# Optimization experiments

Hardware: AMD Instinct MI355X
Metric: run time of the kernel (lower is better)

## Reference

```python
import jax, jax.numpy as jnp
import numpy as np

IN_FEATURES = 4096
OUT_FEATURES = 11008
N_TOKENS = 32


def setup_inputs() -> dict:
    key = jax.random.key(0)
    k_x, k_w, k_s, k_b = jax.random.split(key, 4)
    x = jax.random.normal(k_x, (N_TOKENS, IN_FEATURES), dtype=jnp.float16)
    # int8 quantized weight, [out_features, in_features]
    qweight = jax.random.randint(k_w, (OUT_FEATURES, IN_FEATURES), -128, 128, dtype=jnp.int8)
    # per-output-channel scales, small positive fp16
    scales = (jax.random.uniform(k_s, (OUT_FEATURES,), dtype=jnp.float32) * 0.01 + 1e-4).astype(jnp.float16)
    bias = (jax.random.normal(k_b, (OUT_FEATURES,), dtype=jnp.float32) * 0.01).astype(jnp.float16)
    return {"x": x, "qweight": qweight, "scales": scales, "bias": bias}


def reference(x, qweight, scales, bias):
    # Dequantize: fp16 weight = int8 * per-row scale  -> [out, in]
    w = (qweight.astype(jnp.float16) * scales[:, None]).astype(jnp.float16)
    # out[t, o] = sum_i x[t, i] * w[o, i]
    out = jnp.einsum("ti,oi->to", x, w) + bias[None, :]
    return out.astype(jnp.float16)
```

## Files before the change

kernel.cpp:

```cpp
#include <hip/hip_runtime.h>
#include <hip/hip_bf16.h>


constexpr int IN_F  = 4096;
constexpr int OUT_F = 11008;

typedef short bf16x8 __attribute__((ext_vector_type(8)));
typedef float f32x4  __attribute__((ext_vector_type(4)));

union B8 { bf16x8 v; unsigned u[4]; };

__device__ __forceinline__ unsigned pack2f(float lo, float hi) {
    return __builtin_amdgcn_perm(__float_as_uint(hi),
                                 __float_as_uint(lo),
                                 0x07060302u);
}

__global__ __launch_bounds__(256, 4)
void qlin_kernel(const float* __restrict__ x,
                 const int* __restrict__ w,
                 const float* __restrict__ scales,
                 const float* __restrict__ bias,
                 float* __restrict__ out)
{
    const int lane = threadIdx.x & 63;
    const int wv   = threadIdx.x >> 6;
    const int r    = lane & 15;
    const int q    = lane >> 4;

    const int n0 = blockIdx.x << 4;
    const int kb = wv << 10;

    f32x4 acc0 = {0.f, 0.f, 0.f, 0.f};
    f32x4 acc1 = {0.f, 0.f, 0.f, 0.f};

    const float* xp0 = x + r * IN_F + kb + q * 8;
    const float* xp1 = xp0 + 16 * IN_F;
    const int* wp = w + (size_t)(n0 + r) * IN_F + kb + q * 8;

    #pragma unroll 2
    for (int kk = 0; kk < 1024; kk += 32) {
        float4 xa = *reinterpret_cast<const float4*>(xp0 + kk);
        float4 xb = *reinterpret_cast<const float4*>(xp0 + kk + 4);
        float4 xc = *reinterpret_cast<const float4*>(xp1 + kk);
        float4 xd = *reinterpret_cast<const float4*>(xp1 + kk + 4);
        int4   qa = *reinterpret_cast<const int4*>(wp + kk);
        int4   qb = *reinterpret_cast<const int4*>(wp + kk + 4);

        B8 a0, a1, bb;
        a0.u[0] = pack2f(xa.x, xa.y);  a0.u[1] = pack2f(xa.z, xa.w);
        a0.u[2] = pack2f(xb.x, xb.y);  a0.u[3] = pack2f(xb.z, xb.w);
        a1.u[0] = pack2f(xc.x, xc.y);  a1.u[1] = pack2f(xc.z, xc.w);
        a1.u[2] = pack2f(xd.x, xd.y);  a1.u[3] = pack2f(xd.z, xd.w);
        bb.u[0] = pack2f((float)qa.x, (float)qa.y);
        bb.u[1] = pack2f((float)qa.z, (float)qa.w);
        bb.u[2] = pack2f((float)qb.x, (float)qb.y);
        bb.u[3] = pack2f((float)qb.z, (float)qb.w);

        acc0 = __builtin_amdgcn_mfma_f32_16x16x32_bf16(a0.v, bb.v, acc0, 0, 0, 0);
        acc1 = __builtin_amdgcn_mfma_f32_16x16x32_bf16(a1.v, bb.v, acc1, 0, 0, 0);
    }

    __shared__ float red[3][2][4][64];
    if (wv > 0) {
        #pragma unroll
        for (int i = 0; i < 4; ++i) {
            red[wv - 1][0][i][lane] = acc0[i];
            red[wv - 1][1][i][lane] = acc1[i];
        }
    }
    __syncthreads();
    if (wv == 0) {
        #pragma unroll
        for (int j = 0; j < 3; ++j) {
            #pragma unroll
            for (int i = 0; i < 4; ++i) {
                acc0[i] += red[j][0][i][lane];
                acc1[i] += red[j][1][i][lane];
            }
        }
        const int n = n0 + r;
        const float s = scales[n];
        const float b = bias[n];
        #pragma unroll
        for (int i = 0; i < 4; ++i) {
            out[(q * 4 + i) * OUT_F + n]      = acc0[i] * s + b;
            out[(16 + q * 4 + i) * OUT_F + n] = acc1[i] * s + b;
        }
    }
}

extern "C" void kernel_launch(void* const* d_in, const int* in_sizes, int n_in,
                              void* d_out, int out_size, void* d_ws, size_t ws_size,
                              hipStream_t stream) {
    const float* x      = (const float*)d_in[0];
    const int*   w      = (const int*)d_in[1];
    const float* scales = (const float*)d_in[2];
    const float* bias   = (const float*)d_in[3];
    float*       out    = (float*)d_out;

    qlin_kernel<<<dim3(OUT_F / 16), dim3(256), 0, stream>>>(x, w, scales, bias, out);
}
```

Baseline: 276.1 us.

## Pre-convert activations to bf16 in a prologue kernel and split K across eight waves

Adds a small kernel that converts x from fp32 to packed bf16 into workspace once. The main kernel then loads bf16 vectors directly instead of re-reading fp32 x and packing it in every block, which halves activation traffic and removes per-block conversion ALU work. Blocks grow to 512 threads with K split across 8 waves, and the LDS reduction widens to 7 partial sums. The cost is an extra kernel launch and a larger cross-wave reduction.

```diff
diff --git a/kernel.cpp b/kernel.cpp
--- a/kernel.cpp
+++ b/kernel.cpp
@@ -2,8 +2,9 @@
 #include <hip/hip_bf16.h>
 
 
-constexpr int IN_F  = 4096;
-constexpr int OUT_F = 11008;
+constexpr int IN_F   = 4096;
+constexpr int OUT_F  = 11008;
+constexpr int KSLICE = IN_F / 8;
 
 typedef short bf16x8 __attribute__((ext_vector_type(8)));
 typedef float f32x4  __attribute__((ext_vector_type(4)));
@@ -16,8 +17,16 @@
                                  0x07060302u);
 }
 
-__global__ __launch_bounds__(256, 4)
-void qlin_kernel(const float* __restrict__ x,
+__global__ __launch_bounds__(256)
+void xconv_kernel(const float* __restrict__ x, unsigned* __restrict__ xb) {
+    const int i = (blockIdx.x * 256 + threadIdx.x) * 4;
+    float4 v = *reinterpret_cast<const float4*>(x + i);
+    xb[i / 2]     = pack2f(v.x, v.y);
+    xb[i / 2 + 1] = pack2f(v.z, v.w);
+}
+
+__global__ __launch_bounds__(512, 4)
+void qlin_kernel(const unsigned short* __restrict__ xb,
                  const int* __restrict__ w,
                  const float* __restrict__ scales,
                  const float* __restrict__ bias,
@@ -29,39 +38,31 @@
     const int q    = lane >> 4;
 
     const int n0 = blockIdx.x << 4;
-    const int kb = wv << 10;
+    const int kb = wv * KSLICE;
 
     f32x4 acc0 = {0.f, 0.f, 0.f, 0.f};
     f32x4 acc1 = {0.f, 0.f, 0.f, 0.f};
 
-    const float* xp0 = x + r * IN_F + kb + q * 8;
-    const float* xp1 = xp0 + 16 * IN_F;
+    const unsigned short* xp0 = xb + r * IN_F + kb + q * 8;
+    const unsigned short* xp1 = xp0 + 16 * IN_F;
     const int* wp = w + (size_t)(n0 + r) * IN_F + kb + q * 8;
 
-    #pragma unroll 2
-    for (int kk = 0; kk < 1024; kk += 32) {
-        float4 xa = *reinterpret_cast<const float4*>(xp0 + kk);
-        float4 xb = *reinterpret_cast<const float4*>(xp0 + kk + 4);
-        float4 xc = *reinterpret_cast<const float4*>(xp1 + kk);
-        float4 xd = *reinterpret_cast<const float4*>(xp1 + kk + 4);
+    #pragma unroll 4
+    for (int kk = 0; kk < KSLICE; kk += 32) {
+        bf16x8 a0 = *reinterpret_cast<const bf16x8*>(xp0 + kk);
+        bf16x8 a1 = *reinterpret_cast<const bf16x8*>(xp1 + kk);
         int4   qa = *reinterpret_cast<const int4*>(wp + kk);
         int4   qb = *reinterpret_cast<const int4*>(wp + kk + 4);
-
-        B8 a0, a1, bb;
-        a0.u[0] = pack2f(xa.x, xa.y);  a0.u[1] = pack2f(xa.z, xa.w);
-        a0.u[2] = pack2f(xb.x, xb.y);  a0.u[3] = pack2f(xb.z, xb.w);
-        a1.u[0] = pack2f(xc.x, xc.y);  a1.u[1] = pack2f(xc.z, xc.w);
-        a1.u[2] = pack2f(xd.x, xd.y);  a1.u[3] = pack2f(xd.z, xd.w);
+        B8 bb;
         bb.u[0] = pack2f((float)qa.x, (float)qa.y);
         bb.u[1] = pack2f((float)qa.z, (float)qa.w);
         bb.u[2] = pack2f((float)qb.x, (float)qb.y);
         bb.u[3] = pack2f((float)qb.z, (float)qb.w);
-
-        acc0 = __builtin_amdgcn_mfma_f32_16x16x32_bf16(a0.v, bb.v, acc0, 0, 0, 0);
-        acc1 = __builtin_amdgcn_mfma_f32_16x16x32_bf16(a1.v, bb.v, acc1, 0, 0, 0);
+        acc0 = __builtin_amdgcn_mfma_f32_16x16x32_bf16(a0, bb.v, acc0, 0, 0, 0);
+        acc1 = __builtin_amdgcn_mfma_f32_16x16x32_bf16(a1, bb.v, acc1, 0, 0, 0);
     }
 
-    __shared__ float red[3][2][4][64];
+    __shared__ float red[7][2][4][64];
     if (wv > 0) {
         #pragma unroll
         for (int i = 0; i < 4; ++i) {
@@ -72,7 +73,7 @@
     __syncthreads();
     if (wv == 0) {
         #pragma unroll
-        for (int j = 0; j < 3; ++j) {
+        for (int j = 0; j < 7; ++j) {
             #pragma unroll
             for (int i = 0; i < 4; ++i) {
                 acc0[i] += red[j][0][i][lane];
@@ -98,6 +99,9 @@
     const float* scales = (const float*)d_in[2];
     const float* bias   = (const float*)d_in[3];
     float*       out    = (float*)d_out;
+    unsigned*    xb     = (unsigned*)d_ws;
 
-    qlin_kernel<<<dim3(OUT_F / 16), dim3(256), 0, stream>>>(x, w, scales, bias, out);
+    xconv_kernel<<<dim3(32 * IN_F / (256 * 4)), dim3(256), 0, stream>>>(x, xb);
+    qlin_kernel<<<dim3(OUT_F / 16), dim3(512), 0, stream>>>(
+        (const unsigned short*)xb, w, scales, bias, out);
 }
```

Result: faster. 263.5 us (-4.6%).
